# Optimization experiments

Measured on AMD Instinct MI355X. Metric: run time of the kernel, lower is better.

Reference implementation:

```python
import jax, jax.numpy as jnp
import numpy as np

GROUPS = 32  # min(32, 256//4)
EPS = 1e-5


def setup_inputs() -> dict:
    key = jax.random.key(0)
    ks = jax.random.split(key, 4)
    B, C, H, W = 8, 256, 128, 128
    x = jax.random.normal(ks[0], (B, C, H, W), dtype=jnp.float32)
    gn_w = jnp.ones((C,), dtype=jnp.float32)
    gn_b = jnp.zeros((C,), dtype=jnp.float32)
    qkv_w = jax.random.normal(ks[1], (3 * C, C), dtype=jnp.float32) * (C ** -0.5)
    qkv_b = jnp.zeros((3 * C,), dtype=jnp.float32)
    proj_w = jax.random.normal(ks[2], (C, C), dtype=jnp.float32) * (C ** -0.5)
    proj_b = jnp.zeros((C,), dtype=jnp.float32)
    return {"x": x, "gn_w": gn_w, "gn_b": gn_b, "qkv_w": qkv_w,
            "qkv_b": qkv_b, "proj_w": proj_w, "proj_b": proj_b}


def _group_norm(x, w, b):
    B, C, H, W = x.shape
    xg = x.reshape(B, GROUPS, C // GROUPS, H, W)
    mean = xg.mean(axis=(2, 3, 4), keepdims=True)
    var = xg.var(axis=(2, 3, 4), keepdims=True)
    xg = (xg - mean) * jax.lax.rsqrt(var + EPS)
    x = xg.reshape(B, C, H, W)
    return x * w[None, :, None, None] + b[None, :, None, None]


def reference(x, gn_w, gn_b, qkv_w, qkv_b, proj_w, proj_b):
    B, C, H, W = x.shape
    num_heads = 8
    head_dim = C // num_heads
    scale = head_dim ** -0.5

    h = _group_norm(x, gn_w, gn_b)
    # 1x1 conv == per-pixel matmul over channels
    qkv = jnp.einsum('bchw,oc->bohw', h, qkv_w) + qkv_b[None, :, None, None]
    qkv = qkv.reshape(B, 3, num_heads, head_dim, H * W)
    q, k, v = qkv[:, 0], qkv[:, 1], qkv[:, 2]  # each (B, h, head_dim, HW)
    # Faithful to source: contracts over spatial axis d=HW -> (B,h,hd,hd)
    attn = jnp.einsum('bhid,bhjd->bhij', q, k) * scale
    attn = jax.nn.softmax(attn, axis=-1)
    out = jnp.einsum('bhij,bhjd->bhid', attn, v)  # (B, h, head_dim, HW)
    out = out.reshape(B, C, H, W)
    out = jnp.einsum('bchw,oc->bohw', out, proj_w) + proj_b[None, :, None, None]
    return x + out
```

## Files before the change

### kernel.cpp

```cpp
#include <hip/hip_runtime.h>
#include <stdint.h>

typedef __bf16 bf16;
typedef __attribute__((ext_vector_type(8))) __bf16 bf16x8;
typedef __attribute__((ext_vector_type(4))) float f32x4;

#define S_HW 16384
#define N_C 256

__device__ __forceinline__ f32x4 mfma16(bf16x8 a, bf16x8 b, f32x4 c) {
  return __builtin_amdgcn_mfma_f32_16x16x32_bf16(a, b, c, 0, 0, 0);
}
__device__ __forceinline__ void async_ld16(const bf16* g, bf16* l) {
  __builtin_amdgcn_global_load_lds(
      (const __attribute__((address_space(1))) unsigned int*)g,
      (__attribute__((address_space(3))) unsigned int*)l, 16, 0, 0);
}
__device__ __forceinline__ unsigned short bf2u(bf16 h) {
  union { bf16 h; unsigned short u; } c; c.h = h; return c.u;
}
__device__ __forceinline__ bf16 u2bf(unsigned short u) {
  union { unsigned short u; bf16 h; } c; c.u = u; return c.h;
}

__global__ __launch_bounds__(256) void k_split(
    const float* __restrict__ x, bf16* __restrict__ yhi, bf16* __restrict__ ylo,
    bf16* __restrict__ yt, float* __restrict__ Sx) {
  int b = blockIdx.z, c0 = blockIdx.y * 64, s0 = blockIdx.x * 64;
  __shared__ unsigned T[64][65];
  __shared__ float sxl[256];
  int t = threadIdx.x;
  int cl = t >> 2, sg = t & 3;
  size_t off = (size_t)(b * N_C + c0 + cl) * S_HW + s0 + sg * 16;
  const float* xp = x + off;
  bf16x8 hv[2], lv[2];
  float sum = 0.f;
#pragma unroll
  for (int i2 = 0; i2 < 4; i2++) {
    float4 v = *(const float4*)(xp + i2 * 4);
    float f4[4] = {v.x, v.y, v.z, v.w};
#pragma unroll
    for (int k = 0; k < 4; k++) {
      int i = i2 * 4 + k;
      float fv = f4[k];
      bf16 h = (bf16)fv;
      bf16 l = (bf16)(fv - (float)h);
      hv[i >> 3][i & 7] = h;
      lv[i >> 3][i & 7] = l;
      sum += fv;
      T[sg * 16 + i][cl] = (unsigned)bf2u(h) | ((unsigned)bf2u(l) << 16);
    }
  }
  *(bf16x8*)(yhi + off) = hv[0];
  *(bf16x8*)(yhi + off + 8) = hv[1];
  *(bf16x8*)(ylo + off) = lv[0];
  *(bf16x8*)(ylo + off + 8) = lv[1];
  sxl[t] = sum;
  __syncthreads();
  if (t < 64) {
    float s2 = sxl[t * 4] + sxl[t * 4 + 1] + sxl[t * 4 + 2] + sxl[t * 4 + 3];
    atomicAdd(&Sx[b * N_C + c0 + t], s2);
  }
  int sl = t >> 2, cg = t & 3;
  bf16x8 ho[2], lo2[2];
#pragma unroll
  for (int i = 0; i < 16; i++) {
    unsigned u = T[sl][cg * 16 + i];
    ho[i >> 3][i & 7] = u2bf((unsigned short)(u & 0xffffu));
    lo2[i >> 3][i & 7] = u2bf((unsigned short)(u >> 16));
  }
  size_t tb = (size_t)(b * S_HW + s0 + sl) * 512 + c0 + cg * 16;
  *(bf16x8*)(yt + tb) = ho[0];
  *(bf16x8*)(yt + tb + 8) = ho[1];
  *(bf16x8*)(yt + tb + 256) = lo2[0];
  *(bf16x8*)(yt + tb + 256 + 8) = lo2[1];
}

__global__ __launch_bounds__(512, 2) void k_gram(
    const bf16* __restrict__ yhi, const bf16* __restrict__ ylo,
    float* __restrict__ YG3) {
  constexpr int BK = 64;
  constexpr int NT = 16;
  constexpr int BUF = 256 * BK;
  __shared__ __align__(16) bf16 As[2 * BUF];
  __shared__ __align__(16) bf16 Bs[2 * BUF];
  int kc = blockIdx.x * 1024;
  int nsel = blockIdx.y;
  int b = blockIdx.z;
  int tid = threadIdx.x, lane = tid & 63, wave = tid >> 6;
  int wm = (wave >> 1) * 64, wn = (wave & 1) * 128;
  const bf16* Ab = yhi + (size_t)(b * N_C) * S_HW;
  const bf16* Bb = (nsel == 0 ? yhi : ylo) + (size_t)(b * N_C) * S_HW;
  f32x4 acc[4][8] = {};
  int fm = lane & 15, cs = lane >> 4;

  auto STAGE = [&](int bi, int t) {
    int kt = kc + t * BK;
#pragma unroll
    for (int i = 0; i < 4; i++) {
      int ch = i * 512 + tid;
      int row = ch >> 3, slot = ch & 7;
      int gcol = (slot ^ (row & 7)) * 8;
      async_ld16(Ab + (size_t)row * S_HW + kt + gcol, As + bi * BUF + ch * 8);
      async_ld16(Bb + (size_t)row * S_HW + kt + gcol, Bs + bi * BUF + ch * 8);
    }
  };

  STAGE(0, 0);
  STAGE(1, 1);
  int cur = 0;
  for (int t = 0; t < NT; t++) {
    if (t < NT - 1)
      asm volatile("s_waitcnt vmcnt(8)" ::: "memory");
    else
      asm volatile("s_waitcnt vmcnt(0)" ::: "memory");
    __builtin_amdgcn_s_barrier();
    const bf16* Ap = As + cur * BUF;
    const bf16* Bp = Bs + cur * BUF;
    bf16x8 af[4][2], bfr[8][2];
#pragma unroll
    for (int q = 0; q < 4; q++) {
      int ra = wm + q * 16 + fm;
#pragma unroll
      for (int h = 0; h < 2; h++)
        af[q][h] =
            *(const bf16x8*)(Ap + ra * BK + (((h << 2) | cs) ^ (ra & 7)) * 8);
    }
#pragma unroll
    for (int p = 0; p < 8; p++) {
      int rb = wn + p * 16 + fm;
#pragma unroll
      for (int h = 0; h < 2; h++)
        bfr[p][h] =
            *(const bf16x8*)(Bp + rb * BK + (((h << 2) | cs) ^ (rb & 7)) * 8);
    }
    asm volatile("s_waitcnt lgkmcnt(0)" ::: "memory");
    __builtin_amdgcn_sched_barrier(0);
    __builtin_amdgcn_s_barrier();
    if (t + 2 < NT) STAGE(cur, t + 2);
    __builtin_amdgcn_sched_barrier(0);
    __builtin_amdgcn_s_setprio(1);
#pragma unroll
    for (int q = 0; q < 4; q++)
#pragma unroll
      for (int p = 0; p < 8; p++) {
        acc[q][p] = mfma16(af[q][0], bfr[p][0], acc[q][p]);
        acc[q][p] = mfma16(af[q][1], bfr[p][1], acc[q][p]);
      }
    __builtin_amdgcn_s_setprio(0);
    cur ^= 1;
  }
  int quad = lane >> 4, cn = lane & 15;
  float* yg = YG3 + (size_t)(b * N_C) * 512 + nsel * 256;
#pragma unroll
  for (int q = 0; q < 4; q++)
#pragma unroll
    for (int r = 0; r < 4; r++) {
      int m = wm + q * 16 + quad * 4 + r;
#pragma unroll
      for (int p = 0; p < 8; p++) {
        int n = wn + p * 16 + cn;
        atomicAdd(&yg[(size_t)m * 512 + n], acc[q][p][r]);
      }
    }
}

__global__ __launch_bounds__(256) void k_wkt(const float* __restrict__ qkv_w,
                                             float* __restrict__ WkT) {
  int k = blockIdx.x, j = threadIdx.x;
  WkT[k * 256 + j] = qkv_w[(256 + j) * 256 + k];
}

__global__ __launch_bounds__(256) void k_coefs(
    const float* __restrict__ Sx, const float* __restrict__ YG3,
    const float* __restrict__ gn_w, const float* __restrict__ gn_b,
    const float* __restrict__ qkv_w, const float* __restrict__ qkv_b,
    float* __restrict__ a_, float* __restrict__ bv_, float* __restrict__ u_,
    float* __restrict__ vbe) {
  int b = blockIdx.x, role = blockIdx.y, t = threadIdx.x;
  __shared__ float sxl[256], gxd[256], gm[32], gr[32], sh[256], bl[256];
  __shared__ float ured[64][4];
  sxl[t] = Sx[b * N_C + t];
  gxd[t] = YG3[(size_t)(b * N_C + t) * 512 + t] +
           2.f * YG3[(size_t)(b * N_C + t) * 512 + 256 + t];
  __syncthreads();
  if (t < 32) {
    float s = 0.f, q2 = 0.f;
#pragma unroll
    for (int i = 0; i < 8; i++) { s += sxl[t * 8 + i]; q2 += gxd[t * 8 + i]; }
    float mean = s * (1.f / 131072.f);
    float var = q2 * (1.f / 131072.f) - mean * mean;
    gm[t] = mean;
    gr[t] = 1.f / sqrtf(var + 1e-5f);
  }
  __syncthreads();
  {
    float A = gn_w[t] * gr[t >> 3];
    float B = gn_b[t] - gm[t >> 3] * A;
    bl[t] = B;
    sh[t] = A * sxl[t] + 16384.f * B;
    if (role == 0) {
      a_[b * N_C + t] = A;
      bv_[b * N_C + t] = B;
    }
  }
  __syncthreads();
  if (role == 0) {
    const float* wp = qkv_w + (size_t)(512 + t) * 256;
    float acc = 0.f;
    for (int c = 0; c < 256; c++) acc += wp[c] * bl[c];
    vbe[b * N_C + t] = acc + qkv_b[512 + t];
  } else {
    int r = (role - 1) * 64 + (t >> 2);
    int seg = (t & 3) * 64;
    const float* wp = qkv_w + (size_t)r * 256 + seg;
    float p = 0.f;
    for (int c = 0; c < 64; c++) p += wp[c] * sh[seg + c];
    ured[t >> 2][t & 3] = p;
    __syncthreads();
    if (t < 64)
      u_[b * 512 + (role - 1) * 64 + t] =
          ured[t][0] + ured[t][1] + ured[t][2] + ured[t][3];
  }
}

__global__ __launch_bounds__(256) void k_t1(
    const float* __restrict__ YG3, const float* __restrict__ WkT,
    const float* __restrict__ a_, const float* __restrict__ bv_,
    const float* __restrict__ Sx, float* __restrict__ T1) {
  int tile = blockIdx.x, b = blockIdx.y;
  int i0 = (tile >> 2) * 64, j0 = (tile & 3) * 64;
  __shared__ float As[64][69];
  __shared__ float Bs[64][69];
  __shared__ float al[256], bl[256], sxl[256];
  int t = threadIdx.x;
  al[t] = a_[b * N_C + t];
  bl[t] = bv_[b * N_C + t];
  sxl[t] = Sx[b * N_C + t];
  int cl = t >> 2, qq = (t & 3) * 16;
  int kk = t >> 2, jj = (t & 3) * 16;
  int ti = t >> 4, tj = t & 15;
  float acc[4][4] = {};
  for (int kc = 0; kc < 256; kc += 64) {
    {
      const float* yg = YG3 + (size_t)(b * N_C + i0 + cl) * 512 + kc + qq;
#pragma unroll
      for (int i = 0; i < 16; i++) As[cl][qq + i] = yg[i] + yg[256 + i];
    }
    __syncthreads();
    {
      int cp = kc + kk;
      const float* ygp = YG3 + (size_t)(b * N_C + cp) * 512 + 256 + i0 + jj;
#pragma unroll
      for (int i = 0; i < 16; i++) As[jj + i][kk] += ygp[i];
    }
    __syncthreads();
    {
      int c = i0 + cl;
      float ac = al[c], bc = bl[c], sxc = sxl[c];
#pragma unroll
      for (int i = 0; i < 16; i++) {
        int cp = kc + qq + i;
        As[cl][qq + i] = ac * al[cp] * As[cl][qq + i] + ac * bl[cp] * sxc +
                         bc * al[cp] * sxl[cp] + 16384.f * bc * bl[cp];
      }
    }
    {
      const float* wp = WkT + (size_t)(kc + kk) * 256 + j0 + jj;
#pragma unroll
      for (int i = 0; i < 16; i += 4) {
        float4 v = *(const float4*)(wp + i);
        Bs[kk][jj + i] = v.x; Bs[kk][jj + i + 1] = v.y;
        Bs[kk][jj + i + 2] = v.z; Bs[kk][jj + i + 3] = v.w;
      }
    }
    __syncthreads();
    for (int k = 0; k < 64; k++) {
      float av[4], bv4[4];
#pragma unroll
      for (int ii = 0; ii < 4; ii++) av[ii] = As[ti * 4 + ii][k];
#pragma unroll
      for (int j2 = 0; j2 < 4; j2++) bv4[j2] = Bs[k][tj * 4 + j2];
#pragma unroll
      for (int ii = 0; ii < 4; ii++)
#pragma unroll
        for (int j2 = 0; j2 < 4; j2++) acc[ii][j2] += av[ii] * bv4[j2];
    }
    __syncthreads();
  }
#pragma unroll
  for (int ii = 0; ii < 4; ii++)
#pragma unroll
    for (int j2 = 0; j2 < 4; j2++)
      T1[(size_t)(b * N_C + i0 + ti * 4 + ii) * 256 + j0 + tj * 4 + j2] =
          acc[ii][j2];
}

__global__ __launch_bounds__(256) void k_logits(
    const float* __restrict__ T1, const float* __restrict__ qkv_w,
    const float* __restrict__ qkv_b, const float* __restrict__ u_,
    float* __restrict__ attn) {
  int h = blockIdx.x, b = blockIdx.y;
  __shared__ float Tc[64][33];
  __shared__ float Wql[32][65];
  __shared__ float Ll[32][33];
  __shared__ float uq[32], uk[32], bq[32], bk[32];
  int t = threadIdx.x;
  if (t < 32) {
    uq[t] = u_[b * 512 + h * 32 + t];
    uk[t] = u_[b * 512 + 256 + h * 32 + t];
    bq[t] = qkv_b[h * 32 + t];
    bk[t] = qkv_b[256 + h * 32 + t];
  }
  int i = t & 31, jg = t >> 5;
  float acc[4] = {};
  for (int cc = 0; cc < 256; cc += 64) {
    {
      int c_l = t >> 2, seg = (t & 3) * 8;
      const float* tp = T1 + (size_t)(b * N_C + cc + c_l) * 256 + h * 32 + seg;
      float4 v0 = *(const float4*)tp, v1 = *(const float4*)(tp + 4);
      Tc[c_l][seg] = v0.x; Tc[c_l][seg + 1] = v0.y;
      Tc[c_l][seg + 2] = v0.z; Tc[c_l][seg + 3] = v0.w;
      Tc[c_l][seg + 4] = v1.x; Tc[c_l][seg + 5] = v1.y;
      Tc[c_l][seg + 6] = v1.z; Tc[c_l][seg + 7] = v1.w;
      int row = t >> 3, seg2 = (t & 7) * 8;
      const float* wp = qkv_w + (size_t)(h * 32 + row) * 256 + cc + seg2;
      float4 w0 = *(const float4*)wp, w1 = *(const float4*)(wp + 4);
      Wql[row][seg2] = w0.x; Wql[row][seg2 + 1] = w0.y;
      Wql[row][seg2 + 2] = w0.z; Wql[row][seg2 + 3] = w0.w;
      Wql[row][seg2 + 4] = w1.x; Wql[row][seg2 + 5] = w1.y;
      Wql[row][seg2 + 6] = w1.z; Wql[row][seg2 + 7] = w1.w;
    }
    __syncthreads();
    for (int c = 0; c < 64; c++) {
      float w = Wql[i][c];
#pragma unroll
      for (int j2 = 0; j2 < 4; j2++) acc[j2] += w * Tc[c][jg * 4 + j2];
    }
    __syncthreads();
  }
  const float scale = 0.17677669529663687f;
#pragma unroll
  for (int j2 = 0; j2 < 4; j2++) {
    int j = jg * 4 + j2;
    Ll[i][j] = scale * (acc[j2] + bq[i] * uk[j] + bk[j] * uq[i] +
                        16384.f * bq[i] * bk[j]);
  }
  __syncthreads();
  if (t < 32) {
    float m = -1e30f;
    for (int j = 0; j < 32; j++) m = fmaxf(m, Ll[t][j]);
    float e[32], s = 0.f;
    for (int j = 0; j < 32; j++) { e[j] = expf(Ll[t][j] - m); s += e[j]; }
    float inv = 1.f / s;
    float* ap = attn + (size_t)((b * 8 + h) * 32 + t) * 32;
    for (int j = 0; j < 32; j++) ap[j] = e[j] * inv;
  }
}

__global__ __launch_bounds__(256) void k_pv(
    const float* __restrict__ proj_w, const float* __restrict__ attn,
    const float* __restrict__ qkv_w, const float* __restrict__ a_,
    const float* __restrict__ vbe, const float* __restrict__ proj_b,
    bf16* __restrict__ FA, float* __restrict__ g_) {
  int tile = blockIdx.x, b = blockIdx.y;
  int i0 = (tile >> 2) * 64, j0 = (tile & 3) * 64;
  __shared__ float As[64][69];
  __shared__ float Bs[64][69];
  __shared__ float At[2][32][33];
  __shared__ float gred[64][4];
  int t = threadIdx.x;
  int cl = t >> 2, qq = (t & 3) * 16;
  int kk = t >> 2, jj = (t & 3) * 16;
  int ti = t >> 4, tj = t & 15;
  float acc[4][4] = {};
  float gacc = 0.f;
  for (int kc = 0; kc < 256; kc += 64) {
    int h0 = kc >> 5;
    __syncthreads();
    {
      const float* ap = attn + (size_t)b * 8192 + h0 * 1024;
#pragma unroll
      for (int i = 0; i < 8; i++) {
        int idx = t * 8 + i;
        At[idx >> 10][(idx >> 5) & 31][idx & 31] = ap[idx];
      }
      const float* wp = qkv_w + (size_t)(512 + kc + kk) * 256 + j0 + jj;
#pragma unroll
      for (int i = 0; i < 16; i += 4) {
        float4 v = *(const float4*)(wp + i);
        Bs[kk][jj + i] = v.x; Bs[kk][jj + i + 1] = v.y;
        Bs[kk][jj + i + 2] = v.z; Bs[kk][jj + i + 3] = v.w;
      }
    }
    __syncthreads();
    {
      int hl = qq >> 5;
      int jbase = qq & 31;
      const float* pp = proj_w + (size_t)(i0 + cl) * 256 + (h0 + hl) * 32;
      float pr[32];
#pragma unroll
      for (int i = 0; i < 32; i += 4) {
        float4 v = *(const float4*)(pp + i);
        pr[i] = v.x; pr[i + 1] = v.y; pr[i + 2] = v.z; pr[i + 3] = v.w;
      }
#pragma unroll
      for (int i = 0; i < 16; i++) {
        int jm = jbase + i;
        float s = 0.f;
#pragma unroll
        for (int ii = 0; ii < 32; ii++) s += pr[ii] * At[hl][ii][jm];
        As[cl][qq + i] = s;
        gacc += s * vbe[b * N_C + kc + qq + i];
      }
    }
    __syncthreads();
    for (int k = 0; k < 64; k++) {
      float av[4], bv4[4];
#pragma unroll
      for (int ii = 0; ii < 4; ii++) av[ii] = As[ti * 4 + ii][k];
#pragma unroll
      for (int j2 = 0; j2 < 4; j2++) bv4[j2] = Bs[k][tj * 4 + j2];
#pragma unroll
      for (int ii = 0; ii < 4; ii++)
#pragma unroll
        for (int j2 = 0; j2 < 4; j2++) acc[ii][j2] += av[ii] * bv4[j2];
    }
  }
  __syncthreads();
  gred[cl][t & 3] = gacc;
  __syncthreads();
  if ((tile & 3) == 0 && t < 64)
    g_[b * N_C + i0 + t] =
        gred[t][0] + gred[t][1] + gred[t][2] + gred[t][3] + proj_b[i0 + t];
  float a4[4];
  {
    float4 v = *(const float4*)(a_ + b * N_C + j0 + tj * 4);
    a4[0] = v.x; a4[1] = v.y; a4[2] = v.z; a4[3] = v.w;
  }
#pragma unroll
  for (int ii = 0; ii < 4; ii++) {
    int row = i0 + ti * 4 + ii;
#pragma unroll
    for (int j2 = 0; j2 < 4; j2++) {
      int col = j0 + tj * 4 + j2;
      float f = acc[ii][j2] * a4[j2] + (row == col ? 1.0f : 0.0f);
      bf16 hi = (bf16)f;
      bf16 lo = (bf16)(f - (float)hi);
      FA[(size_t)(b * N_C + row) * 512 + col] = hi;
      FA[(size_t)(b * N_C + row) * 512 + 256 + col] = lo;
    }
  }
}

__global__ __launch_bounds__(512) void k_final(
    const bf16* __restrict__ FA, const bf16* __restrict__ yt,
    const float* __restrict__ g_, float* __restrict__ out) {
  constexpr int BK = 64;
  constexpr int NT = 12;
  constexpr int BUFA = 256 * BK;
  constexpr int BUFB = 128 * BK;
  __shared__ __align__(16) bf16 As[3 * BUFA];
  __shared__ __align__(16) bf16 Bs[3 * BUFB];
  int b = blockIdx.z, n0 = blockIdx.x * 128;
  int tid = threadIdx.x, lane = tid & 63, wave = tid >> 6;
  int wm = (wave >> 1) * 64, wn = (wave & 1) * 64;
  const bf16* Ab = FA + (size_t)b * N_C * 512;
  const bf16* Bb = yt + (size_t)(b * S_HW + n0) * 512;
  f32x4 acc[4][4] = {};
  int fm = lane & 15, cs = lane >> 4;

  auto STAGE = [&](int bi, int t) {
    int kt = t * BK;
    int ka = (kt < 512) ? kt : kt - 512;
    int kb = (kt < 256) ? kt : kt - 256;
#pragma unroll
    for (int i = 0; i < 4; i++) {
      int ch = i * 512 + tid;
      int row = ch >> 3, slot = ch & 7;
      int gcol = (slot ^ (row & 7)) * 8;
      async_ld16(Ab + (size_t)row * 512 + ka + gcol,
                 As + bi * BUFA + ch * 8);
    }
#pragma unroll
    for (int i = 0; i < 2; i++) {
      int ch = i * 512 + tid;
      int row = ch >> 3, slot = ch & 7;
      int gcol = (slot ^ (row & 7)) * 8;
      async_ld16(Bb + (size_t)row * 512 + kb + gcol,
                 Bs + bi * BUFB + ch * 8);
    }
  };

  STAGE(0, 0);
  STAGE(1, 1);
  STAGE(2, 2);
  int bi = 0;
  for (int t = 0; t < NT - 2; t++) {
    asm volatile("s_waitcnt vmcnt(12)" ::: "memory");
    __builtin_amdgcn_s_barrier();
    const bf16* Ap = As + bi * BUFA;
    const bf16* Bp = Bs + bi * BUFB;
    bf16x8 af[4][2], bfr[4][2];
#pragma unroll
    for (int q = 0; q < 4; q++) {
      int ra = wm + q * 16 + fm;
      int rb = wn + q * 16 + fm;
#pragma unroll
      for (int h = 0; h < 2; h++) {
        af[q][h] = *(const bf16x8*)(Ap + ra * BK +
                                    (((h << 2) | cs) ^ (ra & 7)) * 8);
        bfr[q][h] = *(const bf16x8*)(Bp + rb * BK +
                                     (((h << 2) | cs) ^ (rb & 7)) * 8);
      }
    }
    asm volatile("s_waitcnt lgkmcnt(0)" ::: "memory");
    __builtin_amdgcn_sched_barrier(0);
    __builtin_amdgcn_s_barrier();
    if (t + 3 < NT) STAGE(bi, t + 3);
    __builtin_amdgcn_sched_barrier(0);
    __builtin_amdgcn_s_setprio(1);
#pragma unroll
    for (int ti = 0; ti < 4; ti++)
#pragma unroll
      for (int tj = 0; tj < 4; tj++) {
        acc[ti][tj] = mfma16(af[ti][0], bfr[tj][0], acc[ti][tj]);
        acc[ti][tj] = mfma16(af[ti][1], bfr[tj][1], acc[ti][tj]);
      }
    __builtin_amdgcn_s_setprio(0);
    bi = (bi == 2) ? 0 : bi + 1;
  }
#pragma unroll
  for (int pe = 0; pe < 2; pe++) {
    if (pe == 0)
      asm volatile("s_waitcnt vmcnt(6)" ::: "memory");
    else
      asm volatile("s_waitcnt vmcnt(0)" ::: "memory");
    __builtin_amdgcn_s_barrier();
    const bf16* Ap = As + bi * BUFA;
    const bf16* Bp = Bs + bi * BUFB;
    bf16x8 af[4][2], bfr[4][2];
#pragma unroll
    for (int q = 0; q < 4; q++) {
      int ra = wm + q * 16 + fm;
      int rb = wn + q * 16 + fm;
#pragma unroll
      for (int h = 0; h < 2; h++) {
        af[q][h] = *(const bf16x8*)(Ap + ra * BK +
                                    (((h << 2) | cs) ^ (ra & 7)) * 8);
        bfr[q][h] = *(const bf16x8*)(Bp + rb * BK +
                                     (((h << 2) | cs) ^ (rb & 7)) * 8);
      }
    }
#pragma unroll
    for (int ti = 0; ti < 4; ti++)
#pragma unroll
      for (int tj = 0; tj < 4; tj++) {
        acc[ti][tj] = mfma16(af[ti][0], bfr[tj][0], acc[ti][tj]);
        acc[ti][tj] = mfma16(af[ti][1], bfr[tj][1], acc[ti][tj]);
      }
    bi = (bi == 2) ? 0 : bi + 1;
  }
  int quad = lane >> 4, cn = lane & 15;
#pragma unroll
  for (int ti = 0; ti < 4; ti++)
#pragma unroll
    for (int r = 0; r < 4; r++) {
      int row = wm + ti * 16 + quad * 4 + r;
      float gb = g_[b * N_C + row];
#pragma unroll
      for (int tj = 0; tj < 4; tj++) {
        int col = n0 + wn + tj * 16 + cn;
        size_t idx = (size_t)(b * N_C + row) * S_HW + col;
        out[idx] = acc[ti][tj][r] + gb;
      }
    }
}

extern "C" void kernel_launch(void* const* d_in, const int* in_sizes, int n_in,
                              void* d_out, int out_size, void* d_ws,
                              size_t ws_size, hipStream_t stream) {
  const float* x = (const float*)d_in[0];
  const float* gn_w = (const float*)d_in[1];
  const float* gn_b = (const float*)d_in[2];
  const float* qkv_w = (const float*)d_in[3];
  const float* qkv_b = (const float*)d_in[4];
  const float* proj_w = (const float*)d_in[5];
  const float* proj_b = (const float*)d_in[6];
  float* out = (float*)d_out;

  const size_t MB = 1ull << 20;
  char* ws = (char*)d_ws;
  bf16* ylo = (bf16*)ws;
  bf16* yt = (bf16*)(ws + 64 * MB);
  float* YG3 = (float*)(ws + 192 * MB);
  bf16* FA = (bf16*)(ws + 194 * MB);
  float* WkT = (float*)(ws + 196 * MB);
  float* attn = (float*)(ws + 196 * MB + 256 * 1024);
  float* Sx = (float*)(ws + 196 * MB + 512 * 1024);
  float* a_ = (float*)(ws + 196 * MB + 520 * 1024);
  float* bv_ = (float*)(ws + 196 * MB + 528 * 1024);
  float* u_ = (float*)(ws + 196 * MB + 536 * 1024);
  float* vbe = (float*)(ws + 196 * MB + 552 * 1024);
  float* g_ = (float*)(ws + 196 * MB + 560 * 1024);
  float* T1 = (float*)(ws + 198 * MB);
  bf16* yhi = (bf16*)d_out;

  if (ws_size < 200 * MB) return;

  hipMemsetAsync(YG3, 0, 4 * MB + 520 * 1024, stream);
  k_split<<<dim3(256, 4, 8), 256, 0, stream>>>(x, yhi, ylo, yt, Sx);
  k_gram<<<dim3(16, 2, 8), 512, 0, stream>>>(yhi, ylo, YG3);
  k_wkt<<<256, 256, 0, stream>>>(qkv_w, WkT);
  k_coefs<<<dim3(8, 9), 256, 0, stream>>>(Sx, YG3, gn_w, gn_b, qkv_w, qkv_b,
                                          a_, bv_, u_, vbe);
  k_t1<<<dim3(16, 8), 256, 0, stream>>>(YG3, WkT, a_, bv_, Sx, T1);
  k_logits<<<dim3(8, 8), 256, 0, stream>>>(T1, qkv_w, qkv_b, u_, attn);
  k_pv<<<dim3(16, 8), 256, 0, stream>>>(proj_w, attn, qkv_w, a_, vbe, proj_b,
                                        FA, g_);
  k_final<<<dim3(128, 1, 8), 512, 0, stream>>>(FA, yt, g_, out);
}
```

Baseline: 514.9 us.

## Drop transposed activation copy; transpose yhi/ylo in registers inside final GEMM

k_split no longer writes the transposed hi/lo copy (yt), which saves a 64 MB write and the LDS transpose. k_final now reads the channel-major yhi/ylo directly, packing pairs of channels in registers and writing them into a swizzled single LDS B buffer each k-step. The cost is an extra barrier and sync per iteration, plus a B prefetch only one step ahead instead of a 3-stage async pipeline, so the GEMM may stall more. yhi also moves from the output buffer into workspace.

```diff
diff --git a/kernel.cpp b/kernel.cpp
--- a/kernel.cpp
+++ b/kernel.cpp
@@ -4,6 +4,7 @@
 typedef __bf16 bf16;
 typedef __attribute__((ext_vector_type(8))) __bf16 bf16x8;
 typedef __attribute__((ext_vector_type(4))) float f32x4;
+typedef __attribute__((ext_vector_type(4))) unsigned u32x4;
 
 #define S_HW 16384
 #define N_C 256
@@ -19,15 +20,11 @@
 __device__ __forceinline__ unsigned short bf2u(bf16 h) {
   union { bf16 h; unsigned short u; } c; c.h = h; return c.u;
 }
-__device__ __forceinline__ bf16 u2bf(unsigned short u) {
-  union { unsigned short u; bf16 h; } c; c.u = u; return c.h;
-}
 
 __global__ __launch_bounds__(256) void k_split(
     const float* __restrict__ x, bf16* __restrict__ yhi, bf16* __restrict__ ylo,
-    bf16* __restrict__ yt, float* __restrict__ Sx) {
+    float* __restrict__ Sx) {
   int b = blockIdx.z, c0 = blockIdx.y * 64, s0 = blockIdx.x * 64;
-  __shared__ unsigned T[64][65];
   __shared__ float sxl[256];
   int t = threadIdx.x;
   int cl = t >> 2, sg = t & 3;
@@ -48,7 +45,6 @@
       hv[i >> 3][i & 7] = h;
       lv[i >> 3][i & 7] = l;
       sum += fv;
-      T[sg * 16 + i][cl] = (unsigned)bf2u(h) | ((unsigned)bf2u(l) << 16);
     }
   }
   *(bf16x8*)(yhi + off) = hv[0];
@@ -61,19 +57,6 @@
     float s2 = sxl[t * 4] + sxl[t * 4 + 1] + sxl[t * 4 + 2] + sxl[t * 4 + 3];
     atomicAdd(&Sx[b * N_C + c0 + t], s2);
   }
-  int sl = t >> 2, cg = t & 3;
-  bf16x8 ho[2], lo2[2];
-#pragma unroll
-  for (int i = 0; i < 16; i++) {
-    unsigned u = T[sl][cg * 16 + i];
-    ho[i >> 3][i & 7] = u2bf((unsigned short)(u & 0xffffu));
-    lo2[i >> 3][i & 7] = u2bf((unsigned short)(u >> 16));
-  }
-  size_t tb = (size_t)(b * S_HW + s0 + sl) * 512 + c0 + cg * 16;
-  *(bf16x8*)(yt + tb) = ho[0];
-  *(bf16x8*)(yt + tb + 8) = ho[1];
-  *(bf16x8*)(yt + tb + 256) = lo2[0];
-  *(bf16x8*)(yt + tb + 256 + 8) = lo2[1];
 }
 
 __global__ __launch_bounds__(512, 2) void k_gram(
@@ -454,53 +437,70 @@
 }
 
 __global__ __launch_bounds__(512) void k_final(
-    const bf16* __restrict__ FA, const bf16* __restrict__ yt,
-    const float* __restrict__ g_, float* __restrict__ out) {
+    const bf16* __restrict__ FA, const bf16* __restrict__ yhi,
+    const bf16* __restrict__ ylo, const float* __restrict__ g_,
+    float* __restrict__ out) {
   constexpr int BK = 64;
   constexpr int NT = 12;
   constexpr int BUFA = 256 * BK;
-  constexpr int BUFB = 128 * BK;
   __shared__ __align__(16) bf16 As[3 * BUFA];
-  __shared__ __align__(16) bf16 Bs[3 * BUFB];
+  __shared__ __align__(16) bf16 Bs[128 * BK];
   int b = blockIdx.z, n0 = blockIdx.x * 128;
   int tid = threadIdx.x, lane = tid & 63, wave = tid >> 6;
   int wm = (wave >> 1) * 64, wn = (wave & 1) * 64;
   const bf16* Ab = FA + (size_t)b * N_C * 512;
-  const bf16* Bb = yt + (size_t)(b * S_HW + n0) * 512;
   f32x4 acc[4][4] = {};
   int fm = lane & 15, cs = lane >> 4;
-
-  auto STAGE = [&](int bi, int t) {
+  int cp = tid >> 4, sseg = (tid & 15) * 8;
+
+  auto STAGE_A = [&](int bi, int t) {
     int kt = t * BK;
     int ka = (kt < 512) ? kt : kt - 512;
-    int kb = (kt < 256) ? kt : kt - 256;
 #pragma unroll
     for (int i = 0; i < 4; i++) {
       int ch = i * 512 + tid;
       int row = ch >> 3, slot = ch & 7;
       int gcol = (slot ^ (row & 7)) * 8;
-      async_ld16(Ab + (size_t)row * 512 + ka + gcol,
-                 As + bi * BUFA + ch * 8);
-    }
-#pragma unroll
-    for (int i = 0; i < 2; i++) {
-      int ch = i * 512 + tid;
-      int row = ch >> 3, slot = ch & 7;
-      int gcol = (slot ^ (row & 7)) * 8;
-      async_ld16(Bb + (size_t)row * 512 + kb + gcol,
-                 Bs + bi * BUFB + ch * 8);
+      async_ld16(Ab + (size_t)row * 512 + ka + gcol, As + bi * BUFA + ch * 8);
     }
   };
-
-  STAGE(0, 0);
-  STAGE(1, 1);
-  STAGE(2, 2);
-  int bi = 0;
-  for (int t = 0; t < NT - 2; t++) {
-    asm volatile("s_waitcnt vmcnt(12)" ::: "memory");
+  auto BPTR = [&](int t) -> const bf16* {
+    int kt = t * BK;
+    const bf16* src = (kt < 512) ? yhi : ylo;
+    int c0 = (kt < 256) ? kt : ((kt < 512) ? kt - 256 : kt - 512);
+    return src + (size_t)(b * N_C + c0 + 2 * cp) * S_HW + n0 + sseg;
+  };
+
+  u32x4 r0, r1;
+  {
+    const bf16* p = BPTR(0);
+    r0 = *(const u32x4*)p;
+    r1 = *(const u32x4*)(p + S_HW);
+  }
+  STAGE_A(0, 0);
+  STAGE_A(1, 1);
+  STAGE_A(2, 2);
+
+  int slotW = cp >> 2, cw = (cp & 3) * 2;
+  for (int t = 0; t < NT; t++) {
+    if (t == 0)
+      asm volatile("s_waitcnt vmcnt(8)" ::: "memory");
+    else if (t <= 9)
+      asm volatile("s_waitcnt vmcnt(4)" ::: "memory");
+    else
+      asm volatile("s_waitcnt vmcnt(0)" ::: "memory");
     __builtin_amdgcn_s_barrier();
-    const bf16* Ap = As + bi * BUFA;
-    const bf16* Bp = Bs + bi * BUFB;
+#pragma unroll
+    for (int i = 0; i < 8; i++) {
+      int s = sseg + i;
+      int sl2 = slotW ^ (s & 7) ^ ((s >> 3) & 7);
+      unsigned h0 = (((const unsigned*)&r0)[i >> 1] >> ((i & 1) * 16)) & 0xffffu;
+      unsigned h1 = (((const unsigned*)&r1)[i >> 1] >> ((i & 1) * 16)) & 0xffffu;
+      *(unsigned*)(Bs + s * 64 + sl2 * 8 + cw) = h0 | (h1 << 16);
+    }
+    asm volatile("s_waitcnt lgkmcnt(0)" ::: "memory");
+    __builtin_amdgcn_s_barrier();
+    const bf16* Ap = As + (t % 3) * BUFA;
     bf16x8 af[4][2], bfr[4][2];
 #pragma unroll
     for (int q = 0; q < 4; q++) {
@@ -508,16 +508,21 @@
       int rb = wn + q * 16 + fm;
 #pragma unroll
       for (int h = 0; h < 2; h++) {
-        af[q][h] = *(const bf16x8*)(Ap + ra * BK +
-                                    (((h << 2) | cs) ^ (ra & 7)) * 8);
-        bfr[q][h] = *(const bf16x8*)(Bp + rb * BK +
-                                     (((h << 2) | cs) ^ (rb & 7)) * 8);
+        int slot = (h << 2) | cs;
+        af[q][h] = *(const bf16x8*)(Ap + ra * BK + (slot ^ (ra & 7)) * 8);
+        bfr[q][h] = *(const bf16x8*)(
+            Bs + rb * 64 + (slot ^ (rb & 7) ^ ((rb >> 3) & 7)) * 8);
       }
     }
     asm volatile("s_waitcnt lgkmcnt(0)" ::: "memory");
     __builtin_amdgcn_sched_barrier(0);
     __builtin_amdgcn_s_barrier();
-    if (t + 3 < NT) STAGE(bi, t + 3);
+    if (t + 1 < NT) {
+      const bf16* p = BPTR(t + 1);
+      r0 = *(const u32x4*)p;
+      r1 = *(const u32x4*)(p + S_HW);
+    }
+    if (t + 3 < NT) STAGE_A((t + 3) % 3, t + 3);
     __builtin_amdgcn_sched_barrier(0);
     __builtin_amdgcn_s_setprio(1);
 #pragma unroll
@@ -528,38 +533,6 @@
         acc[ti][tj] = mfma16(af[ti][1], bfr[tj][1], acc[ti][tj]);
       }
     __builtin_amdgcn_s_setprio(0);
-    bi = (bi == 2) ? 0 : bi + 1;
-  }
-#pragma unroll
-  for (int pe = 0; pe < 2; pe++) {
-    if (pe == 0)
-      asm volatile("s_waitcnt vmcnt(6)" ::: "memory");
-    else
-      asm volatile("s_waitcnt vmcnt(0)" ::: "memory");
-    __builtin_amdgcn_s_barrier();
-    const bf16* Ap = As + bi * BUFA;
-    const bf16* Bp = Bs + bi * BUFB;
-    bf16x8 af[4][2], bfr[4][2];
-#pragma unroll
-    for (int q = 0; q < 4; q++) {
-      int ra = wm + q * 16 + fm;
-      int rb = wn + q * 16 + fm;
-#pragma unroll
-      for (int h = 0; h < 2; h++) {
-        af[q][h] = *(const bf16x8*)(Ap + ra * BK +
-                                    (((h << 2) | cs) ^ (ra & 7)) * 8);
-        bfr[q][h] = *(const bf16x8*)(Bp + rb * BK +
-                                     (((h << 2) | cs) ^ (rb & 7)) * 8);
-      }
-    }
-#pragma unroll
-    for (int ti = 0; ti < 4; ti++)
-#pragma unroll
-      for (int tj = 0; tj < 4; tj++) {
-        acc[ti][tj] = mfma16(af[ti][0], bfr[tj][0], acc[ti][tj]);
-        acc[ti][tj] = mfma16(af[ti][1], bfr[tj][1], acc[ti][tj]);
-      }
-    bi = (bi == 2) ? 0 : bi + 1;
   }
   int quad = lane >> 4, cn = lane & 15;
 #pragma unroll
@@ -592,7 +565,7 @@
   const size_t MB = 1ull << 20;
   char* ws = (char*)d_ws;
   bf16* ylo = (bf16*)ws;
-  bf16* yt = (bf16*)(ws + 64 * MB);
+  bf16* yhi = (bf16*)(ws + 64 * MB);
   float* YG3 = (float*)(ws + 192 * MB);
   bf16* FA = (bf16*)(ws + 194 * MB);
   float* WkT = (float*)(ws + 196 * MB);
@@ -604,12 +577,11 @@
   float* vbe = (float*)(ws + 196 * MB + 552 * 1024);
   float* g_ = (float*)(ws + 196 * MB + 560 * 1024);
   float* T1 = (float*)(ws + 198 * MB);
-  bf16* yhi = (bf16*)d_out;
 
   if (ws_size < 200 * MB) return;
 
   hipMemsetAsync(YG3, 0, 4 * MB + 520 * 1024, stream);
-  k_split<<<dim3(256, 4, 8), 256, 0, stream>>>(x, yhi, ylo, yt, Sx);
+  k_split<<<dim3(256, 4, 8), 256, 0, stream>>>(x, yhi, ylo, Sx);
   k_gram<<<dim3(16, 2, 8), 512, 0, stream>>>(yhi, ylo, YG3);
   k_wkt<<<256, 256, 0, stream>>>(qkv_w, WkT);
   k_coefs<<<dim3(8, 9), 256, 0, stream>>>(Sx, YG3, gn_w, gn_b, qkv_w, qkv_b,
@@ -618,5 +590,5 @@
   k_logits<<<dim3(8, 8), 256, 0, stream>>>(T1, qkv_w, qkv_b, u_, attn);
   k_pv<<<dim3(16, 8), 256, 0, stream>>>(proj_w, attn, qkv_w, a_, vbe, proj_b,
                                         FA, g_);
-  k_final<<<dim3(128, 1, 8), 512, 0, stream>>>(FA, yt, g_, out);
-}
+  k_final<<<dim3(128, 1, 8), 512, 0, stream>>>(FA, yhi, ylo, g_, out);
+}
```

Measured after the change: 502.0 us. -2.5%, faster.
